# Kernel tuning notes

Hardware: AMD Instinct MI355X
Metric: run time of the kernel (lower is better)

Reference implementation:

```python
import jax, jax.numpy as jnp
import numpy as np

B, N, D_PAIR, D_HID = 1, 512, 128, 128

def _layernorm(x, gamma, beta, eps=1e-5):
    mu = jnp.mean(x, axis=-1, keepdims=True)
    var = jnp.mean(jnp.square(x - mu), axis=-1, keepdims=True)
    return (x - mu) * jax.lax.rsqrt(var + eps) * gamma + beta

def setup_inputs() -> dict:
    key = jax.random.key(0)
    ks = jax.random.split(key, 8)
    s = 0.02  # small init scale for weights
    return {
        "z": jax.random.normal(ks[0], (B, N, N, D_PAIR), dtype=jnp.float32),
        "mask": jnp.ones((B, N, N), dtype=jnp.float32),
        "w_ab_p": jax.random.normal(ks[1], (2 * D_HID, D_PAIR), dtype=jnp.float32) * s,
        "b_ab_p": jnp.zeros((2 * D_HID,), dtype=jnp.float32),
        "w_ab_g": jax.random.normal(ks[2], (2 * D_HID, D_PAIR), dtype=jnp.float32) * s,
        "b_ab_g": jnp.zeros((2 * D_HID,), dtype=jnp.float32),
        "w_g": jax.random.normal(ks[3], (D_PAIR, D_PAIR), dtype=jnp.float32) * s,
        "b_g": jnp.zeros((D_PAIR,), dtype=jnp.float32),
        "w_z": jax.random.normal(ks[4], (D_PAIR, D_HID), dtype=jnp.float32) * s,
        "b_z": jnp.zeros((D_PAIR,), dtype=jnp.float32),
        "ln_in_g": jnp.ones((D_PAIR,), dtype=jnp.float32),
        "ln_in_b": jnp.zeros((D_PAIR,), dtype=jnp.float32),
        "ln_out_g": jnp.ones((D_HID,), dtype=jnp.float32),
        "ln_out_b": jnp.zeros((D_HID,), dtype=jnp.float32),
    }

def reference(z, mask, w_ab_p, b_ab_p, w_ab_g, b_ab_g, w_g, b_g, w_z, b_z,
              ln_in_g, ln_in_b, ln_out_g, ln_out_b):
    z_ = _layernorm(z, ln_in_g, ln_in_b)                      # [B,N,N,c_z]
    ab = (z_ @ w_ab_p.T + b_ab_p) * jax.nn.sigmoid(z_ @ w_ab_g.T + b_ab_g)
    ab = ab * mask[..., None]                                 # [B,N,N,2h]
    a, b = jnp.split(ab, 2, axis=-1)                          # [B,N,N,h] each
    # outgoing=True: sum over k of a[i,k,d]*b[j,k,d]
    x = jnp.einsum('bikd,bjkd->bijd', a, b)                   # [B,N,N,h]
    g = jax.nn.sigmoid(z @ w_g.T + b_g)                       # [B,N,N,c_z]
    out = g * (_layernorm(x, ln_out_g, ln_out_b) @ w_z.T + b_z)
    return out
```

## Files before the change

kernel.cpp:

```cpp
#include <hip/hip_runtime.h>
#include <stdint.h>

#define NSEQ 512
#define DPAIR 128
#define NN (NSEQ*NSEQ)
#define LDPAD 136

typedef unsigned short u16;
typedef __attribute__((ext_vector_type(8))) short bf16x8;
typedef __attribute__((ext_vector_type(4))) float f32x4;

__device__ __forceinline__ float bf2f(u16 h){ return __uint_as_float(((uint32_t)h)<<16); }
__device__ __forceinline__ u16 f2bf(float f){
  uint32_t u = __float_as_uint(f);
  u += 0x7fffu + ((u>>16)&1u);
  return (u16)(u>>16);
}
__device__ __forceinline__ uint32_t cvtpk(float lo, float hi){
  uint32_t r;
  asm("v_cvt_pk_bf16_f32 %0, %1, %2" : "=v"(r) : "v"(lo), "v"(hi));
  return r;
}
__device__ __forceinline__ float sigmoidf_(float x){ return 1.0f/(1.0f+__expf(-x)); }

__device__ __forceinline__ void stage_w64(const float* __restrict__ src, u16* wb, int t){
  const float4* ws = (const float4*)src;
  #pragma unroll
  for (int i=0;i<8;i++){
    int e4 = i*256 + t; int r = e4>>5, c4 = e4&31;
    float4 v = ws[e4];
    uint2 pk;
    pk.x = cvtpk(v.x, v.y);
    pk.y = cvtpk(v.z, v.w);
    *(uint2*)&wb[r*LDPAD + c4*4] = pk;
  }
}

__device__ __forceinline__ void gemm_64x64(const u16* A, const u16* W,
                                           int wm, int wn, int fr, int fq,
                                           f32x4 (&acc)[2][2]){
  #pragma unroll
  for (int kk=0;kk<4;kk++){
    bf16x8 aF[2], bF[2];
    #pragma unroll
    for (int mi=0;mi<2;mi++) aF[mi] = *(const bf16x8*)(A + (wm+mi*16+fr)*LDPAD + kk*32 + fq*8);
    #pragma unroll
    for (int ni=0;ni<2;ni++) bF[ni] = *(const bf16x8*)(W + (wn+ni*16+fr)*LDPAD + kk*32 + fq*8);
    #pragma unroll
    for (int mi=0;mi<2;mi++)
      #pragma unroll
      for (int ni=0;ni<2;ni++)
        acc[mi][ni] = __builtin_amdgcn_mfma_f32_16x16x32_bf16(aF[mi], bF[ni], acc[mi][ni], 0, 0, 0);
  }
}

__global__ __launch_bounds__(256) void k1_proj(
    const float* __restrict__ z, const float* __restrict__ mask,
    const float* __restrict__ w_ab_p, const float* __restrict__ b_ab_p,
    const float* __restrict__ w_ab_g, const float* __restrict__ b_ab_g,
    const float* __restrict__ w_g, const float* __restrict__ b_g,
    const float* __restrict__ ln_g, const float* __restrict__ ln_b,
    u16* __restrict__ a_t, u16* __restrict__ b_t, u16* __restrict__ g_out)
{
  __shared__ u16 zr[64*LDPAD];
  __shared__ u16 wb[64*LDPAD];
  __shared__ float lng[DPAIR], lnb[DPAIR], msk[64];

  const int t = threadIdx.x;
  const int p0 = blockIdx.x * 64;
  const int lane = t & 63, wv = t >> 6;
  const int wm = (wv >> 1) * 32, wn = (wv & 1) * 32;
  const int fr = lane & 15, fq = lane >> 4;

  if (t < DPAIR){ lng[t] = ln_g[t]; lnb[t] = ln_b[t]; }
  else if (t < DPAIR + 64) msk[t - DPAIR] = mask[p0 + t - DPAIR];

  {
    const float4* zs = (const float4*)(z + (size_t)p0 * DPAIR);
    #pragma unroll
    for (int i=0;i<8;i++){
      int e4 = i*256 + t; int pos = e4>>5, c4 = e4&31;
      float4 v = zs[e4];
      uint2 pk;
      pk.x = cvtpk(v.x, v.y);
      pk.y = cvtpk(v.z, v.w);
      *(uint2*)&zr[pos*LDPAD + c4*4] = pk;
    }
  }
  stage_w64(w_g, wb, t);
  __syncthreads();
  #pragma unroll
  for (int h=0; h<2; h++){
    f32x4 acc[2][2] = {};
    gemm_64x64(zr, wb, wm, wn, fr, fq, acc);
    #pragma unroll
    for (int mi=0;mi<2;mi++)
      #pragma unroll
      for (int ni=0;ni<2;ni++){
        int ng = h*64 + wn + ni*16 + fr;
        float bg = b_g[ng];
        #pragma unroll
        for (int r=0;r<4;r++){
          int pos = wm + mi*16 + fq*4 + r;
          g_out[(size_t)(p0+pos)*DPAIR + ng] = f2bf(sigmoidf_(acc[mi][ni][r] + bg));
        }
      }
    __syncthreads();
    if (h == 0){
      stage_w64(w_g + 64*DPAIR, wb, t);
      __syncthreads();
    }
  }

  {
    int pos = t>>2, q = t&3;
    float s=0.f, s2=0.f;
    #pragma unroll
    for (int j=0;j<32;j++){ float v = bf2f(zr[pos*LDPAD + q*32 + j]); s += v; s2 += v*v; }
    s  += __shfl_xor(s, 1);  s2 += __shfl_xor(s2, 1);
    s  += __shfl_xor(s, 2);  s2 += __shfl_xor(s2, 2);
    float mu  = s * (1.f/128.f);
    float var = s2 * (1.f/128.f) - mu*mu;
    float rs  = rsqrtf(var + 1e-5f);
    #pragma unroll
    for (int j=0;j<32;j++){
      int c = q*32 + j;
      float v = bf2f(zr[pos*LDPAD + c]);
      zr[pos*LDPAD + c] = f2bf((v - mu)*rs*lng[c] + lnb[c]);
    }
  }
  __syncthreads();

  for (int nt=0; nt<4; nt++){
    stage_w64(w_ab_p + (size_t)nt*64*DPAIR, wb, t);
    __syncthreads();
    f32x4 accP[2][2] = {};
    gemm_64x64(zr, wb, wm, wn, fr, fq, accP);
    __syncthreads();
    stage_w64(w_ab_g + (size_t)nt*64*DPAIR, wb, t);
    __syncthreads();
    f32x4 accG[2][2] = {};
    gemm_64x64(zr, wb, wm, wn, fr, fq, accG);
    u16* dst = (nt < 2) ? a_t : b_t;
    int dbase = (nt & 1) * 64;
    #pragma unroll
    for (int mi=0;mi<2;mi++){
      int posb = wm + mi*16 + fq*4;
      #pragma unroll
      for (int ni=0;ni<2;ni++){
        int nl   = wn + ni*16 + fr;
        int ng   = nt*64 + nl;
        int drow = dbase + nl;
        float bp  = b_ab_p[ng];
        float bgv = b_ab_g[ng];
        float v0 = (accP[mi][ni][0]+bp) * sigmoidf_(accG[mi][ni][0]+bgv) * msk[posb+0];
        float v1 = (accP[mi][ni][1]+bp) * sigmoidf_(accG[mi][ni][1]+bgv) * msk[posb+1];
        float v2 = (accP[mi][ni][2]+bp) * sigmoidf_(accG[mi][ni][2]+bgv) * msk[posb+2];
        float v3 = (accP[mi][ni][3]+bp) * sigmoidf_(accG[mi][ni][3]+bgv) * msk[posb+3];
        uint2 pk;
        pk.x = (uint32_t)f2bf(v0) | ((uint32_t)f2bf(v1)<<16);
        pk.y = (uint32_t)f2bf(v2) | ((uint32_t)f2bf(v3)<<16);
        *(uint2*)&dst[(size_t)drow*NN + p0 + posb] = pk;
      }
    }
    __syncthreads();
  }
}

__global__ __launch_bounds__(256) void k2_einsum(
    const u16* __restrict__ a_t, const u16* __restrict__ b_t, u16* __restrict__ x_t)
{
  __shared__ u16 As[128*40];
  __shared__ u16 Bs[128*40];
  const int t = threadIdx.x;
  const int d  = blockIdx.z;
  const int i0 = blockIdx.x * 128;
  const int j0 = blockIdx.y * 128;
  const u16* Ag = a_t + (size_t)d*NN + (size_t)i0*NSEQ;
  const u16* Bg = b_t + (size_t)d*NN + (size_t)j0*NSEQ;

  const int lane = t & 63, wv = t >> 6;
  const int wm = (wv >> 1) * 64, wn = (wv & 1) * 64;
  const int fr = lane & 15, fq = lane >> 4;

  f32x4 acc[4][4] = {};

  for (int k0 = 0; k0 < NSEQ; k0 += 32){
    __syncthreads();
    #pragma unroll
    for (int i=0;i<2;i++){
      int e = i*256 + t; int r = e>>2, c8 = e&3;
      uint4 va = *(const uint4*)(Ag + (size_t)r*NSEQ + k0 + c8*8);
      *(uint4*)&As[r*40 + c8*8] = va;
      uint4 vb = *(const uint4*)(Bg + (size_t)r*NSEQ + k0 + c8*8);
      *(uint4*)&Bs[r*40 + c8*8] = vb;
    }
    __syncthreads();
    bf16x8 aF[4], bF[4];
    #pragma unroll
    for (int mi=0;mi<4;mi++) aF[mi] = *(const bf16x8*)&As[(wm + mi*16 + fr)*40 + fq*8];
    #pragma unroll
    for (int ni=0;ni<4;ni++) bF[ni] = *(const bf16x8*)&Bs[(wn + ni*16 + fr)*40 + fq*8];
    #pragma unroll
    for (int mi=0;mi<4;mi++)
      #pragma unroll
      for (int ni=0;ni<4;ni++)
        acc[mi][ni] = __builtin_amdgcn_mfma_f32_16x16x32_bf16(aF[mi], bF[ni], acc[mi][ni], 0, 0, 0);
  }
  u16* Xg = x_t + (size_t)d*NN;
  #pragma unroll
  for (int mi=0;mi<4;mi++)
    #pragma unroll
    for (int ni=0;ni<4;ni++)
      #pragma unroll
      for (int r=0;r<4;r++){
        int row = i0 + wm + mi*16 + fq*4 + r;
        int col = j0 + wn + ni*16 + fr;
        Xg[(size_t)row*NSEQ + col] = f2bf(acc[mi][ni][r]);
      }
}

__global__ __launch_bounds__(256) void k3_out(
    const u16* __restrict__ x_t, const u16* __restrict__ g_in,
    const float* __restrict__ w_z, const float* __restrict__ b_z,
    const float* __restrict__ ln_g, const float* __restrict__ ln_b,
    float* __restrict__ out)
{
  __shared__ u16 xs[64*LDPAD];
  __shared__ u16 wz[DPAIR*LDPAD];
  __shared__ float lng[DPAIR], lnb[DPAIR], bzs[DPAIR];

  const int t = threadIdx.x;
  const int p0 = blockIdx.x * 64;
  if (t < DPAIR){ lng[t] = ln_g[t]; lnb[t] = ln_b[t]; bzs[t] = b_z[t]; }

  {
    const float4* ws = (const float4*)w_z;
    #pragma unroll
    for (int i=0;i<16;i++){
      int e4 = i*256 + t; int r = e4>>5, c4 = e4&31;
      float4 v = ws[e4];
      uint2 pk;
      pk.x = cvtpk(v.x, v.y);
      pk.y = cvtpk(v.z, v.w);
      *(uint2*)&wz[r*LDPAD + c4*4] = pk;
    }
  }
  {
    #pragma unroll
    for (int i=0;i<8;i++){
      int e = i*256 + t; int dd = e>>4, pc = e&15;
      uint2 v = *(const uint2*)(x_t + (size_t)dd*NN + p0 + pc*4);
      int pb = pc*4;
      xs[(pb+0)*LDPAD + dd] = (u16)(v.x & 0xffffu);
      xs[(pb+1)*LDPAD + dd] = (u16)(v.x >> 16);
      xs[(pb+2)*LDPAD + dd] = (u16)(v.y & 0xffffu);
      xs[(pb+3)*LDPAD + dd] = (u16)(v.y >> 16);
    }
  }
  __syncthreads();
  {
    int pos = t>>2, q = t&3;
    float s=0.f, s2=0.f;
    #pragma unroll
    for (int j=0;j<32;j++){ float v = bf2f(xs[pos*LDPAD + q*32 + j]); s += v; s2 += v*v; }
    s  += __shfl_xor(s, 1);  s2 += __shfl_xor(s2, 1);
    s  += __shfl_xor(s, 2);  s2 += __shfl_xor(s2, 2);
    float mu  = s * (1.f/128.f);
    float var = s2 * (1.f/128.f) - mu*mu;
    float rs  = rsqrtf(var + 1e-5f);
    #pragma unroll
    for (int j=0;j<32;j++){
      int c = q*32 + j;
      float v = bf2f(xs[pos*LDPAD + c]);
      xs[pos*LDPAD + c] = f2bf((v - mu)*rs*lng[c] + lnb[c]);
    }
  }
  __syncthreads();
  const int lane = t & 63, wv = t >> 6;
  const int wm = (wv >> 1) * 32, wn = (wv & 1) * 64;
  const int fr = lane & 15, fq = lane >> 4;
  f32x4 acc[2][4] = {};
  #pragma unroll
  for (int kk=0;kk<4;kk++){
    bf16x8 aF[2], bF[4];
    #pragma unroll
    for (int mi=0;mi<2;mi++) aF[mi] = *(const bf16x8*)&xs[(wm+mi*16+fr)*LDPAD + kk*32 + fq*8];
    #pragma unroll
    for (int ni=0;ni<4;ni++) bF[ni] = *(const bf16x8*)&wz[(wn+ni*16+fr)*LDPAD + kk*32 + fq*8];
    #pragma unroll
    for (int mi=0;mi<2;mi++)
      #pragma unroll
      for (int ni=0;ni<4;ni++)
        acc[mi][ni] = __builtin_amdgcn_mfma_f32_16x16x32_bf16(aF[mi], bF[ni], acc[mi][ni], 0, 0, 0);
  }
  #pragma unroll
  for (int mi=0;mi<2;mi++)
    #pragma unroll
    for (int ni=0;ni<4;ni++)
      #pragma unroll
      for (int r=0;r<4;r++){
        int pos = wm + mi*16 + fq*4 + r;
        int c   = wn + ni*16 + fr;
        float gv = bf2f(g_in[(size_t)(p0+pos)*DPAIR + c]);
        out[(size_t)(p0+pos)*DPAIR + c] = gv * (acc[mi][ni][r] + bzs[c]);
      }
}

extern "C" void kernel_launch(void* const* d_in, const int* in_sizes, int n_in,
                              void* d_out, int out_size, void* d_ws, size_t ws_size,
                              hipStream_t stream)
{
  const float* z        = (const float*)d_in[0];
  const float* mask     = (const float*)d_in[1];
  const float* w_ab_p   = (const float*)d_in[2];
  const float* b_ab_p   = (const float*)d_in[3];
  const float* w_ab_g   = (const float*)d_in[4];
  const float* b_ab_g   = (const float*)d_in[5];
  const float* w_g      = (const float*)d_in[6];
  const float* b_g      = (const float*)d_in[7];
  const float* w_z      = (const float*)d_in[8];
  const float* b_z      = (const float*)d_in[9];
  const float* ln_in_g  = (const float*)d_in[10];
  const float* ln_in_b  = (const float*)d_in[11];
  const float* ln_out_g = (const float*)d_in[12];
  const float* ln_out_b = (const float*)d_in[13];
  float* out = (float*)d_out;

  const size_t plane = (size_t)DPAIR * NN;
  if (ws_size < 4 * plane * sizeof(u16)) return;

  u16* a_t = (u16*)d_ws;
  u16* b_t = a_t + plane;
  u16* g_b = b_t + plane;
  u16* x_t = g_b + plane;

  k1_proj<<<dim3(NN/64), dim3(256), 0, stream>>>(
      z, mask, w_ab_p, b_ab_p, w_ab_g, b_ab_g, w_g, b_g, ln_in_g, ln_in_b, a_t, b_t, g_b);
  k2_einsum<<<dim3(4, 4, DPAIR), dim3(256), 0, stream>>>(a_t, b_t, x_t);
  k3_out<<<dim3(NN/64), dim3(256), 0, stream>>>(x_t, g_b, w_z, b_z, ln_out_g, ln_out_b, out);
}
```

Before: 542.8 us.

## Load projection weights directly from global into MFMA fragments, dropping LDS staging

```diff
diff --git a/kernel.cpp b/kernel.cpp
--- a/kernel.cpp
+++ b/kernel.cpp
@@ -23,35 +23,16 @@
 }
 __device__ __forceinline__ float sigmoidf_(float x){ return 1.0f/(1.0f+__expf(-x)); }
 
-__device__ __forceinline__ void stage_w64(const float* __restrict__ src, u16* wb, int t){
-  const float4* ws = (const float4*)src;
-  #pragma unroll
-  for (int i=0;i<8;i++){
-    int e4 = i*256 + t; int r = e4>>5, c4 = e4&31;
-    float4 v = ws[e4];
-    uint2 pk;
-    pk.x = cvtpk(v.x, v.y);
-    pk.y = cvtpk(v.z, v.w);
-    *(uint2*)&wb[r*LDPAD + c4*4] = pk;
-  }
-}
-
-__device__ __forceinline__ void gemm_64x64(const u16* A, const u16* W,
-                                           int wm, int wn, int fr, int fq,
-                                           f32x4 (&acc)[2][2]){
-  #pragma unroll
-  for (int kk=0;kk<4;kk++){
-    bf16x8 aF[2], bF[2];
-    #pragma unroll
-    for (int mi=0;mi<2;mi++) aF[mi] = *(const bf16x8*)(A + (wm+mi*16+fr)*LDPAD + kk*32 + fq*8);
-    #pragma unroll
-    for (int ni=0;ni<2;ni++) bF[ni] = *(const bf16x8*)(W + (wn+ni*16+fr)*LDPAD + kk*32 + fq*8);
-    #pragma unroll
-    for (int mi=0;mi<2;mi++)
-      #pragma unroll
-      for (int ni=0;ni<2;ni++)
-        acc[mi][ni] = __builtin_amdgcn_mfma_f32_16x16x32_bf16(aF[mi], bF[ni], acc[mi][ni], 0, 0, 0);
-  }
+__device__ __forceinline__ bf16x8 ldw(const float* __restrict__ w, int row, int koff){
+  const float* p = w + (size_t)row*DPAIR + koff;
+  float4 w0 = *(const float4*)p;
+  float4 w1 = *(const float4*)(p+4);
+  union { uint32_t u[4]; bf16x8 v; } bu;
+  bu.u[0] = cvtpk(w0.x, w0.y);
+  bu.u[1] = cvtpk(w0.z, w0.w);
+  bu.u[2] = cvtpk(w1.x, w1.y);
+  bu.u[3] = cvtpk(w1.z, w1.w);
+  return bu.v;
 }
 
 __global__ __launch_bounds__(256) void k1_proj(
@@ -63,7 +44,6 @@
     u16* __restrict__ a_t, u16* __restrict__ b_t, u16* __restrict__ g_out)
 {
   __shared__ u16 zr[64*LDPAD];
-  __shared__ u16 wb[64*LDPAD];
   __shared__ float lng[DPAIR], lnb[DPAIR], msk[64];
 
   const int t = threadIdx.x;
@@ -71,6 +51,7 @@
   const int lane = t & 63, wv = t >> 6;
   const int wm = (wv >> 1) * 32, wn = (wv & 1) * 32;
   const int fr = lane & 15, fq = lane >> 4;
+  const int koff = fq*8;
 
   if (t < DPAIR){ lng[t] = ln_g[t]; lnb[t] = ln_b[t]; }
   else if (t < DPAIR + 64) msk[t - DPAIR] = mask[p0 + t - DPAIR];
@@ -87,12 +68,24 @@
       *(uint2*)&zr[pos*LDPAD + c4*4] = pk;
     }
   }
-  stage_w64(w_g, wb, t);
-  __syncthreads();
+  __syncthreads();
+
   #pragma unroll
   for (int h=0; h<2; h++){
     f32x4 acc[2][2] = {};
-    gemm_64x64(zr, wb, wm, wn, fr, fq, acc);
+    #pragma unroll
+    for (int kk=0;kk<4;kk++){
+      bf16x8 aF[2];
+      #pragma unroll
+      for (int mi=0;mi<2;mi++) aF[mi] = *(const bf16x8*)&zr[(wm+mi*16+fr)*LDPAD + kk*32 + koff];
+      #pragma unroll
+      for (int ni=0;ni<2;ni++){
+        bf16x8 bF = ldw(w_g, h*64 + wn + ni*16 + fr, kk*32 + koff);
+        #pragma unroll
+        for (int mi=0;mi<2;mi++)
+          acc[mi][ni] = __builtin_amdgcn_mfma_f32_16x16x32_bf16(aF[mi], bF, acc[mi][ni], 0, 0, 0);
+      }
+    }
     #pragma unroll
     for (int mi=0;mi<2;mi++)
       #pragma unroll
@@ -105,12 +98,8 @@
           g_out[(size_t)(p0+pos)*DPAIR + ng] = f2bf(sigmoidf_(acc[mi][ni][r] + bg));
         }
       }
-    __syncthreads();
-    if (h == 0){
-      stage_w64(w_g + 64*DPAIR, wb, t);
-      __syncthreads();
-    }
-  }
+  }
+  __syncthreads();
 
   {
     int pos = t>>2, q = t&3;
@@ -132,15 +121,24 @@
   __syncthreads();
 
   for (int nt=0; nt<4; nt++){
-    stage_w64(w_ab_p + (size_t)nt*64*DPAIR, wb, t);
-    __syncthreads();
-    f32x4 accP[2][2] = {};
-    gemm_64x64(zr, wb, wm, wn, fr, fq, accP);
-    __syncthreads();
-    stage_w64(w_ab_g + (size_t)nt*64*DPAIR, wb, t);
-    __syncthreads();
-    f32x4 accG[2][2] = {};
-    gemm_64x64(zr, wb, wm, wn, fr, fq, accG);
+    f32x4 accP[2][2] = {}, accG[2][2] = {};
+    #pragma unroll
+    for (int kk=0;kk<4;kk++){
+      bf16x8 aF[2];
+      #pragma unroll
+      for (int mi=0;mi<2;mi++) aF[mi] = *(const bf16x8*)&zr[(wm+mi*16+fr)*LDPAD + kk*32 + koff];
+      #pragma unroll
+      for (int ni=0;ni<2;ni++){
+        int row = nt*64 + wn + ni*16 + fr;
+        bf16x8 bP = ldw(w_ab_p, row, kk*32 + koff);
+        bf16x8 bG = ldw(w_ab_g, row, kk*32 + koff);
+        #pragma unroll
+        for (int mi=0;mi<2;mi++){
+          accP[mi][ni] = __builtin_amdgcn_mfma_f32_16x16x32_bf16(aF[mi], bP, accP[mi][ni], 0, 0, 0);
+          accG[mi][ni] = __builtin_amdgcn_mfma_f32_16x16x32_bf16(aF[mi], bG, accG[mi][ni], 0, 0, 0);
+        }
+      }
+    }
     u16* dst = (nt < 2) ? a_t : b_t;
     int dbase = (nt & 1) * 64;
     #pragma unroll
@@ -158,12 +156,11 @@
         float v2 = (accP[mi][ni][2]+bp) * sigmoidf_(accG[mi][ni][2]+bgv) * msk[posb+2];
         float v3 = (accP[mi][ni][3]+bp) * sigmoidf_(accG[mi][ni][3]+bgv) * msk[posb+3];
         uint2 pk;
-        pk.x = (uint32_t)f2bf(v0) | ((uint32_t)f2bf(v1)<<16);
-        pk.y = (uint32_t)f2bf(v2) | ((uint32_t)f2bf(v3)<<16);
+        pk.x = cvtpk(v0, v1);
+        pk.y = cvtpk(v2, v3);
         *(uint2*)&dst[(size_t)drow*NN + p0 + posb] = pk;
       }
     }
-    __syncthreads();
   }
 }
 
```

Result: slower. 701.9 us (+29.3%).
